# Kernel tuning notes

Measured on AMD Instinct MI355X. Metric: run time of the kernel, lower is better.

The kernel has to match this reference:

```python
import jax, jax.numpy as jnp
import numpy as np

H = 128  # hidden size
D = 257  # input size


def _lstm(x, h0, c0, Wih, Whh, bih, bhh):
    """Single-layer batch-first LSTM, PyTorch gate order (i, f, g, o).
    x: [N, T, D_in]; h0, c0: [N, H]. Returns (ys [N,T,H], hT, cT)."""
    # Precompute the input contribution for all timesteps at once.
    pre = jnp.einsum('ntd,gd->ntg', x, Wih) + bih + bhh  # [N, T, 4H]

    def step(carry, g_t):
        h, c = carry
        gates = g_t + h @ Whh.T  # [N, 4H]
        i, f, g, o = jnp.split(gates, 4, axis=-1)
        c = jax.nn.sigmoid(f) * c + jax.nn.sigmoid(i) * jnp.tanh(g)
        h = jax.nn.sigmoid(o) * jnp.tanh(c)
        return (h, c), h

    (hT, cT), ys = jax.lax.scan(step, (h0, c0), jnp.swapaxes(pre, 0, 1))
    return jnp.swapaxes(ys, 0, 1), hT, cT


def setup_inputs() -> dict:
    key = jax.random.key(0)
    ks = jax.random.split(key, 12)
    N, T = 64, 1000
    s1 = 1.0 / np.sqrt(H)
    inp = {
        'x': jax.random.normal(ks[0], (N, T, D), jnp.float32),
        'in_states': jax.random.normal(ks[1], (1, 4 * N, H), jnp.float32),
        'Wih1': jax.random.uniform(ks[2], (4 * H, D), jnp.float32, -s1, s1),
        'Whh1': jax.random.uniform(ks[3], (4 * H, H), jnp.float32, -s1, s1),
        'bih1': jax.random.uniform(ks[4], (4 * H,), jnp.float32, -s1, s1),
        'bhh1': jax.random.uniform(ks[5], (4 * H,), jnp.float32, -s1, s1),
        'Wih2': jax.random.uniform(ks[6], (4 * H, H), jnp.float32, -s1, s1),
        'Whh2': jax.random.uniform(ks[7], (4 * H, H), jnp.float32, -s1, s1),
        'bih2': jax.random.uniform(ks[8], (4 * H,), jnp.float32, -s1, s1),
        'bhh2': jax.random.uniform(ks[9], (4 * H,), jnp.float32, -s1, s1),
        'Wd': jax.random.uniform(ks[10], (D, H), jnp.float32, -s1, s1),
        'bd': jax.random.uniform(ks[11], (D,), jnp.float32, -s1, s1),
    }
    return inp


def reference(x, in_states, Wih1, Whh1, bih1, bhh1, Wih2, Whh2, bih2, bhh2, Wd, bd):
    # in_states: [1, 4N, H] -> four [1, N, H] chunks: h1, c1, h2, c2
    h1_in, c1_in, h2_in, c2_in = jnp.split(in_states, 4, axis=1)
    x1, h1, c1 = _lstm(x, h1_in[0], c1_in[0], Wih1, Whh1, bih1, bhh1)
    # dropout is identity in eval/streaming inference
    x2, h2, c2 = _lstm(x1, h2_in[0], c2_in[0], Wih2, Whh2, bih2, bhh2)
    mask = jax.nn.sigmoid(jnp.einsum('nth,dh->ntd', x2, Wd) + bd)
    out_states = jnp.concatenate([h1[None], c1[None], h2[None], c2[None]], axis=1)
    return mask, out_states
```

## Files before the change

### kernel.cpp

```cpp
#include <hip/hip_runtime.h>
#include <hip/hip_bf16.h>
#include <math.h>

#define NBATCH 64
#define TSEQ   1000
#define DIN    257
#define HID    128
#define GATES  512
#define CH     40
#define NCHUNK 25

typedef _Float16 h2    __attribute__((ext_vector_type(2)));
typedef _Float16 h4    __attribute__((ext_vector_type(4)));
typedef _Float16 half8 __attribute__((ext_vector_type(8)));
typedef float    f32x4 __attribute__((ext_vector_type(4)));

__device__ __forceinline__ float fast_sigmoid(float x) {
    return __builtin_amdgcn_rcpf(1.f + __expf(-x));
}
__device__ __forceinline__ float fast_tanh(float x) {
    const float e = __expf(2.f * x);
    return 1.f - 2.f * __builtin_amdgcn_rcpf(e + 1.f);
}
__device__ __forceinline__ void wait_flag(const int* f, int need) {
    while (__hip_atomic_load(f, __ATOMIC_ACQUIRE, __HIP_MEMORY_SCOPE_AGENT) < need)
        __builtin_amdgcn_s_sleep(2);
}
__device__ __forceinline__ half8 cvt8(const float* p) {
    const float4 a = *(const float4*)p;
    const float4 b = *(const float4*)(p + 4);
    half8 t;
    t[0] = (_Float16)a.x; t[1] = (_Float16)a.y;
    t[2] = (_Float16)a.z; t[3] = (_Float16)a.w;
    t[4] = (_Float16)b.x; t[5] = (_Float16)b.y;
    t[6] = (_Float16)b.z; t[7] = (_Float16)b.w;
    return t;
}

#define BM 128
#define BN 64
#define BK 64
#define LDK 88

template<int ACT>
__global__ __launch_bounds__(256) void gemm_mfma(
    const float* __restrict__ A, const float* __restrict__ W,
    const float* __restrict__ b1, const float* __restrict__ b2,
    float* __restrict__ C, int M, int K, int Ncols)
{
    __shared__ _Float16 As[BM][LDK];
    __shared__ _Float16 Ws[BN][LDK];

    const int tid  = threadIdx.x;
    const int wave = tid >> 6;
    const int lane = tid & 63;
    const int r    = lane & 15;
    const int q    = lane >> 4;
    const int m0   = blockIdx.y * BM;
    const int n0   = blockIdx.x * BN;
    const int wm   = (wave >> 1) * 64;
    const int wn   = (wave & 1) * 32;

    const int r16 = tid >> 4;
    const int c4  = (tid & 15) * 4;

    f32x4 acc[4][2];
#pragma unroll
    for (int i = 0; i < 4; ++i)
#pragma unroll
        for (int j = 0; j < 2; ++j) acc[i][j] = f32x4{0.f, 0.f, 0.f, 0.f};

    for (int kc = 0; kc < K; kc += BK) {
        const int kg = kc + c4;
        const bool vec_ok = (kg + 4 <= K);

#pragma unroll
        for (int it = 0; it < 8; ++it) {
            const int row = it * 16 + r16;
            const float* src = A + (size_t)(m0 + row) * K + kg;
            _Float16 tmp[4];
            if (vec_ok) {
                const float4 u = *(const float4*)src;
                tmp[0] = (_Float16)u.x; tmp[1] = (_Float16)u.y;
                tmp[2] = (_Float16)u.z; tmp[3] = (_Float16)u.w;
            } else {
#pragma unroll
                for (int j = 0; j < 4; ++j)
                    tmp[j] = (kg + j < K) ? (_Float16)src[j] : (_Float16)0.f;
            }
            *(h4*)&As[row][c4] = *(h4*)tmp;
        }
#pragma unroll
        for (int it = 0; it < 4; ++it) {
            const int row  = it * 16 + r16;
            const int wrow = n0 + row;
            _Float16 tmp[4] = {(_Float16)0.f, (_Float16)0.f, (_Float16)0.f, (_Float16)0.f};
            if (wrow < Ncols) {
                const float* src = W + (size_t)wrow * K + kg;
                if (vec_ok) {
                    const float4 u = *(const float4*)src;
                    tmp[0] = (_Float16)u.x; tmp[1] = (_Float16)u.y;
                    tmp[2] = (_Float16)u.z; tmp[3] = (_Float16)u.w;
                } else {
#pragma unroll
                    for (int j = 0; j < 4; ++j)
                        tmp[j] = (kg + j < K) ? (_Float16)src[j] : (_Float16)0.f;
                }
            }
            *(h4*)&Ws[row][c4] = *(h4*)tmp;
        }
        __syncthreads();

#pragma unroll
        for (int s = 0; s < 2; ++s) {
            const int kb = s * 32 + q * 8;
            half8 af[4], wfr[2];
#pragma unroll
            for (int i = 0; i < 4; ++i)
                af[i] = *(const half8*)&As[wm + i * 16 + r][kb];
#pragma unroll
            for (int j = 0; j < 2; ++j)
                wfr[j] = *(const half8*)&Ws[wn + j * 16 + r][kb];
#pragma unroll
            for (int i = 0; i < 4; ++i)
#pragma unroll
                for (int j = 0; j < 2; ++j)
                    acc[i][j] = __builtin_amdgcn_mfma_f32_16x16x32_f16(
                        af[i], wfr[j], acc[i][j], 0, 0, 0);
        }
        __syncthreads();
    }

#pragma unroll
    for (int i = 0; i < 4; ++i) {
#pragma unroll
        for (int j = 0; j < 2; ++j) {
            const int col = n0 + wn + j * 16 + r;
            if (col < Ncols) {
                const float bias = b1[col] + (b2 ? b2[col] : 0.f);
#pragma unroll
                for (int reg = 0; reg < 4; ++reg) {
                    const int row = m0 + wm + i * 16 + q * 4 + reg;
                    float v = acc[i][j][reg] + bias;
                    if (ACT == 1) v = fast_sigmoid(v);
                    C[(size_t)row * Ncols + col] = v;
                }
            }
        }
    }
}

__global__ __launch_bounds__(256, 1) void lstm_mega(
    const float* __restrict__ pre1, const float* __restrict__ states_in,
    const float* __restrict__ Whh1, const float* __restrict__ Whh2,
    const float* __restrict__ Wih2, const float* __restrict__ bih2,
    const float* __restrict__ bhh2,
    _Float16* __restrict__ h1g,
    float* __restrict__ h2seq,
    float* __restrict__ states_out, int* __restrict__ flags)
{
    const int layer = blockIdx.x >> 6;
    const int n     = blockIdx.x & 63;
    const int tid   = threadIdx.x;
    const int w     = tid >> 6;
    const int lane  = tid & 63;
    const int r     = lane & 15;
    const int q     = lane >> 4;
    const int b     = q & 1;
    const int j     = 32 * w + 16 * b + r;
    const int h_row0 = layer ? 128 : 0;

    __shared__ __align__(16) _Float16 hbuf[2][HID];
    __shared__ __align__(16) float pre2ck[CH][GATES + 4];

    const float* Whh = layer ? Whh2 : Whh1;
    half8 wf[4][2][4];
#pragma unroll
    for (int g = 0; g < 4; ++g)
#pragma unroll
        for (int b2 = 0; b2 < 2; ++b2) {
            const float* src = Whh + (size_t)(128 * g + 32 * w + 16 * b2 + r) * HID + q * 8;
#pragma unroll
            for (int s = 0; s < 4; ++s) wf[g][b2][s] = cvt8(src + s * 32);
        }

    half8 wih[8][4];
    float bias2v[8];
    if (layer == 1) {
#pragma unroll
        for (int fi = 0; fi < 8; ++fi) {
            const int row = 128 * w + 16 * fi + r;
            const float* src = Wih2 + (size_t)row * HID + q * 8;
#pragma unroll
            for (int s = 0; s < 4; ++s) wih[fi][s] = cvt8(src + s * 32);
            bias2v[fi] = bih2[row] + bhh2[row];
        }
    }

    float c_r = states_in[(size_t)(h_row0 + 64 + n) * HID + j];
    if (tid < HID)
        hbuf[0][tid] = (_Float16)states_in[(size_t)(h_row0 + n) * HID + tid];
    __syncthreads();

    const float* pre_n = pre1 + (size_t)n * TSEQ * GATES;
    float pc0 = 0.f, pc1 = 0.f, pc2 = 0.f, pc3 = 0.f;
    float pn0 = 0.f, pn1 = 0.f, pn2 = 0.f, pn3 = 0.f;
    if (layer == 0) {
        pc0 = pre_n[j];           pc1 = pre_n[j + 128];
        pc2 = pre_n[j + 256];     pc3 = pre_n[j + 384];
        pn0 = pre_n[GATES + j];       pn1 = pre_n[GATES + j + 128];
        pn2 = pre_n[GATES + j + 256]; pn3 = pre_n[GATES + j + 384];
    }

    const f32x4 Z = {0.f, 0.f, 0.f, 0.f};
    int cur = 0, ts = 0, ck = 0;

    for (int t = 0; t < TSEQ; ++t) {
        if (layer == 1 && ts == 0) {
            wait_flag(flags + n, ck + 1);
            const _Float16* hbase = h1g + ((size_t)n * TSEQ + (size_t)ck * CH) * HID;
#pragma unroll
            for (int mt = 0; mt < 3; ++mt) {
                const int mrow = (mt < 2) ? (mt * 16 + r) : (32 + (r & 7));
                const _Float16* src = hbase + (size_t)mrow * HID + q * 8;
                half8 ax[4];
#pragma unroll
                for (int s = 0; s < 4; ++s)
                    ax[s] = *(const half8*)(src + s * 32);
                f32x4 gacc[8];
#pragma unroll
                for (int fi = 0; fi < 8; ++fi)
                    gacc[fi] = __builtin_amdgcn_mfma_f32_16x16x32_f16(
                        ax[0], wih[fi][0], Z, 0, 0, 0);
#pragma unroll
                for (int s = 1; s < 4; ++s)
#pragma unroll
                    for (int fi = 0; fi < 8; ++fi)
                        gacc[fi] = __builtin_amdgcn_mfma_f32_16x16x32_f16(
                            ax[s], wih[fi][s], gacc[fi], 0, 0, 0);
                if (mt < 2 || q < 2) {
#pragma unroll
                    for (int fi = 0; fi < 8; ++fi)
#pragma unroll
                        for (int reg = 0; reg < 4; ++reg)
                            pre2ck[mt * 16 + 4 * q + reg][128 * w + 16 * fi + r] =
                                gacc[fi][reg] + bias2v[fi];
                }
            }
            __syncthreads();
        }

        float p0, p1, p2, p3;
        if (layer == 0) {
            p0 = pc0; p1 = pc1; p2 = pc2; p3 = pc3;
            pc0 = pn0; pc1 = pn1; pc2 = pn2; pc3 = pn3;
            if (t + 2 < TSEQ) {
                const float* pp = pre_n + (size_t)(t + 2) * GATES + j;
                pn0 = pp[0]; pn1 = pp[128]; pn2 = pp[256]; pn3 = pp[384];
            }
        } else {
            p0 = pre2ck[ts][j];
            p1 = pre2ck[ts][j + 128];
            p2 = pre2ck[ts][j + 256];
            p3 = pre2ck[ts][j + 384];
        }

        half8 hx[4];
#pragma unroll
        for (int s = 0; s < 4; ++s)
            hx[s] = *(const half8*)&hbuf[cur][s * 32 + q * 8];

        f32x4 acc[4][2];
#pragma unroll
        for (int g = 0; g < 4; ++g)
#pragma unroll
            for (int b2 = 0; b2 < 2; ++b2)
                acc[g][b2] = __builtin_amdgcn_mfma_f32_16x16x32_f16(
                    hx[0], wf[g][b2][0], Z, 0, 0, 0);
#pragma unroll
        for (int s = 1; s < 4; ++s)
#pragma unroll
            for (int g = 0; g < 4; ++g)
#pragma unroll
                for (int b2 = 0; b2 < 2; ++b2)
                    acc[g][b2] = __builtin_amdgcn_mfma_f32_16x16x32_f16(
                        hx[s], wf[g][b2][s], acc[g][b2], 0, 0, 0);

        const float A0 = (b ? acc[0][1][0] : acc[0][0][0]) + p0;
        const float A1 = (b ? acc[1][1][0] : acc[1][0][0]) + p1;
        const float A2 = (b ? acc[2][1][0] : acc[2][0][0]) + p2;
        const float A3 = (b ? acc[3][1][0] : acc[3][0][0]) + p3;

        const float gi = fast_sigmoid(A0);
        const float gf = fast_sigmoid(A1);
        const float gg = fast_tanh(A2);
        const float go = fast_sigmoid(A3);

        const float cn = gf * c_r + gi * gg;
        const float hh = go * fast_tanh(cn);
        c_r = cn;

        if (q < 2) {
            hbuf[cur ^ 1][j] = (_Float16)hh;
            if (t == TSEQ - 1)
                states_out[(size_t)(h_row0 + 64 + n) * HID + j] = cn;
        } else {
            if (layer == 0)
                h1g[((size_t)n * TSEQ + t) * HID + j] = (_Float16)hh;
            else
                h2seq[((size_t)n * TSEQ + t) * HID + j] = hh;
            if (t == TSEQ - 1)
                states_out[(size_t)(h_row0 + n) * HID + j] = hh;
        }
        __syncthreads();

        if (layer == 0 && ts == CH - 1 && tid == 0) {
            __threadfence();
            __hip_atomic_store(flags + n, ck + 1,
                               __ATOMIC_RELAXED, __HIP_MEMORY_SCOPE_AGENT);
        }

        if (++ts == CH) { ts = 0; ++ck; }
        cur ^= 1;
    }
}

extern "C" void kernel_launch(void* const* d_in, const int* in_sizes, int n_in,
                              void* d_out, int out_size, void* d_ws, size_t ws_size,
                              hipStream_t stream)
{
    const float* x     = (const float*)d_in[0];
    const float* st_in = (const float*)d_in[1];
    const float* Wih1  = (const float*)d_in[2];
    const float* Whh1  = (const float*)d_in[3];
    const float* bih1  = (const float*)d_in[4];
    const float* bhh1  = (const float*)d_in[5];
    const float* Wih2  = (const float*)d_in[6];
    const float* Whh2  = (const float*)d_in[7];
    const float* bih2  = (const float*)d_in[8];
    const float* bhh2  = (const float*)d_in[9];
    const float* Wd    = (const float*)d_in[10];
    const float* bd    = (const float*)d_in[11];

    float* out_mask   = (float*)d_out;
    float* out_states = (float*)d_out + (size_t)NBATCH * TSEQ * DIN;

    const int M = NBATCH * TSEQ;
    float* bufA = (float*)d_ws;
    float* bufB = bufA + (size_t)M * GATES;

    _Float16* h1g = (_Float16*)out_mask;
    int* flags = (int*)(out_mask + (size_t)NBATCH * TSEQ * DIN) - 64;
    hipMemsetAsync(flags, 0, 64 * sizeof(int), stream);

    gemm_mfma<0><<<dim3(GATES / BN, M / BM), 256, 0, stream>>>(
        x, Wih1, bih1, bhh1, bufA, M, DIN, GATES);

    lstm_mega<<<128, 256, 0, stream>>>(
        bufA, st_in, Whh1, Whh2, Wih2, bih2, bhh2, h1g, bufB, out_states, flags);

    gemm_mfma<1><<<dim3((DIN + BN - 1) / BN, M / BM), 256, 0, stream>>>(
        bufB, Wd, bd, nullptr, out_mask, M, HID, DIN);
}
```

Measured before the change: 1.097 ms.

## Fuse mask projection GEMM into layer-2 LSTM blocks per chunk

Removes the final mask GEMM launch and the fp32 h2 sequence round-trip through global memory. Layer-2 blocks now keep each 40-step chunk of h2 in LDS as fp16, hold an fp16 swizzled copy of Wd in LDS, and compute and store sigmoid masks with MFMA at the start of the next chunk. The h1 staging buffer moves from the output region to workspace, and its stores become nontemporal. The cost is more LDS use and extra work on the layer-2 path. All four waves appear to redo the same mask computation and write identical outputs.

```diff
diff --git a/kernel.cpp b/kernel.cpp
--- a/kernel.cpp
+++ b/kernel.cpp
@@ -155,8 +155,9 @@
     const float* __restrict__ Whh1, const float* __restrict__ Whh2,
     const float* __restrict__ Wih2, const float* __restrict__ bih2,
     const float* __restrict__ bhh2,
+    const float* __restrict__ Wd, const float* __restrict__ bd,
     _Float16* __restrict__ h1g,
-    float* __restrict__ h2seq,
+    float* __restrict__ mask_out,
     float* __restrict__ states_out, int* __restrict__ flags)
 {
     const int layer = blockIdx.x >> 6;
@@ -171,7 +172,9 @@
     const int h_row0 = layer ? 128 : 0;
 
     __shared__ __align__(16) _Float16 hbuf[2][HID];
-    __shared__ __align__(16) float pre2ck[CH][GATES + 4];
+    __shared__ __align__(16) float    pre2ck[CH][GATES + 4];
+    __shared__ __align__(16) _Float16 wd_lds[272][HID];
+    __shared__ __align__(16) _Float16 h2ck[CH][136];
 
     const float* Whh = layer ? Whh2 : Whh1;
     half8 wf[4][2][4];
@@ -194,6 +197,16 @@
 #pragma unroll
             for (int s = 0; s < 4; ++s) wih[fi][s] = cvt8(src + s * 32);
             bias2v[fi] = bih2[row] + bhh2[row];
+        }
+        for (int i = tid; i < 15 * HID; i += 256)
+            wd_lds[257 + (i >> 7)][i & 127] = (_Float16)0.f;
+        for (int i = tid; i < 257 * 32; i += 256) {
+            const int row = i >> 5, c4 = (i & 31) * 4;
+            const float4 u = *(const float4*)(Wd + (size_t)row * HID + c4);
+            _Float16 t4[4] = {(_Float16)u.x, (_Float16)u.y,
+                              (_Float16)u.z, (_Float16)u.w};
+            const int byte = row * 256 + ((c4 * 2) ^ ((row & 7) << 4));
+            *(h4*)((char*)&wd_lds[0][0] + byte) = *(h4*)t4;
         }
     }
 
@@ -213,10 +226,50 @@
     }
 
     const f32x4 Z = {0.f, 0.f, 0.f, 0.f};
+
+    auto mask_fold = [&](int c) {
+#pragma unroll
+        for (int mt = 0; mt < 3; ++mt) {
+            const int mrow = (mt < 2) ? (mt * 16 + r) : (32 + (r & 7));
+            half8 ax[4];
+#pragma unroll
+            for (int s = 0; s < 4; ++s)
+                ax[s] = *(const half8*)&h2ck[mrow][s * 32 + q * 8];
+#pragma unroll
+            for (int fi = 0; fi < 17; ++fi) {
+                const int wrow = 16 * fi + r;
+                half8 wb[4];
+#pragma unroll
+                for (int s = 0; s < 4; ++s) {
+                    const int byte = wrow * 256 +
+                        ((s * 64 + q * 16) ^ ((wrow & 7) << 4));
+                    wb[s] = *(const half8*)((const char*)&wd_lds[0][0] + byte);
+                }
+                f32x4 g = __builtin_amdgcn_mfma_f32_16x16x32_f16(
+                    ax[0], wb[0], Z, 0, 0, 0);
+#pragma unroll
+                for (int s = 1; s < 4; ++s)
+                    g = __builtin_amdgcn_mfma_f32_16x16x32_f16(
+                        ax[s], wb[s], g, 0, 0, 0);
+                if (wrow < DIN && (mt < 2 || q < 2)) {
+                    const float bias = bd[wrow];
+#pragma unroll
+                    for (int reg = 0; reg < 4; ++reg) {
+                        const int tt = c * CH + mt * 16 + 4 * q + reg;
+                        __builtin_nontemporal_store(
+                            fast_sigmoid(g[reg] + bias),
+                            mask_out + ((size_t)n * TSEQ + tt) * DIN + wrow);
+                    }
+                }
+            }
+        }
+    };
+
     int cur = 0, ts = 0, ck = 0;
 
     for (int t = 0; t < TSEQ; ++t) {
         if (layer == 1 && ts == 0) {
+            if (ck > 0) mask_fold(ck - 1);
             wait_flag(flags + n, ck + 1);
             const _Float16* hbase = h1g + ((size_t)n * TSEQ + (size_t)ck * CH) * HID;
 #pragma unroll
@@ -306,9 +359,10 @@
                 states_out[(size_t)(h_row0 + 64 + n) * HID + j] = cn;
         } else {
             if (layer == 0)
-                h1g[((size_t)n * TSEQ + t) * HID + j] = (_Float16)hh;
+                __builtin_nontemporal_store((_Float16)hh,
+                    &h1g[((size_t)n * TSEQ + t) * HID + j]);
             else
-                h2seq[((size_t)n * TSEQ + t) * HID + j] = hh;
+                h2ck[ts][j] = (_Float16)hh;
             if (t == TSEQ - 1)
                 states_out[(size_t)(h_row0 + n) * HID + j] = hh;
         }
@@ -323,6 +377,8 @@
         if (++ts == CH) { ts = 0; ++ck; }
         cur ^= 1;
     }
+
+    if (layer == 1) mask_fold(NCHUNK - 1);
 }
 
 extern "C" void kernel_launch(void* const* d_in, const int* in_sizes, int n_in,
@@ -349,16 +405,14 @@
     float* bufA = (float*)d_ws;
     float* bufB = bufA + (size_t)M * GATES;
 
-    _Float16* h1g = (_Float16*)out_mask;
-    int* flags = (int*)(out_mask + (size_t)NBATCH * TSEQ * DIN) - 64;
+    _Float16* h1g = (_Float16*)bufB;
+    int* flags = (int*)(bufB + (size_t)M * (HID / 2));
     hipMemsetAsync(flags, 0, 64 * sizeof(int), stream);
 
     gemm_mfma<0><<<dim3(GATES / BN, M / BM), 256, 0, stream>>>(
         x, Wih1, bih1, bhh1, bufA, M, DIN, GATES);
 
     lstm_mega<<<128, 256, 0, stream>>>(
-        bufA, st_in, Whh1, Whh2, Wih2, bih2, bhh2, h1g, bufB, out_states, flags);
-
-    gemm_mfma<1><<<dim3((DIN + BN - 1) / BN, M / BM), 256, 0, stream>>>(
-        bufB, Wd, bd, nullptr, out_mask, M, HID, DIN);
-}
+        bufA, st_in, Whh1, Whh2, Wih2, bih2, bhh2, Wd, bd,
+        h1g, out_mask, out_states, flags);
+}
```

After: 2.050 ms. +86.8%, slower.

## Batch 16 sequences per block and pipeline layer-2 input projection in separate blocks

Applied to the files above, without the earlier changes.

Restructures the recurrent LSTM kernel so each 512-thread block advances 16 batch chains together, using the full 16 rows of each MFMA instead of one sequence per block. A swizzled LDS h buffer avoids bank conflicts. The layer-2 input projection moves into 64 dedicated producer blocks that write pre-activations back into the layer-1 buffer, synchronised through two flag arrays, so the layer-2 recurrence only consumes precomputed values. This cuts per-step work and barrier count per sequence, but adds inter-block flag waits and more global-memory traffic for the layer-2 pre-activations.

```diff
diff --git a/kernel.cpp b/kernel.cpp
--- a/kernel.cpp
+++ b/kernel.cpp
@@ -7,8 +7,9 @@
 #define DIN    257
 #define HID    128
 #define GATES  512
-#define CH     40
+#define CHK    40
 #define NCHUNK 25
+#define GPC    16
 
 typedef _Float16 h2    __attribute__((ext_vector_type(2)));
 typedef _Float16 h4    __attribute__((ext_vector_type(4)));
@@ -150,178 +151,187 @@
     }
 }
 
-__global__ __launch_bounds__(256, 1) void lstm_mega(
-    const float* __restrict__ pre1, const float* __restrict__ states_in,
+__global__ __launch_bounds__(512, 1) void lstm_pipe(
+    float* preA,
+    const float* __restrict__ states_in,
     const float* __restrict__ Whh1, const float* __restrict__ Whh2,
     const float* __restrict__ Wih2, const float* __restrict__ bih2,
     const float* __restrict__ bhh2,
-    _Float16* __restrict__ h1g,
+    _Float16* h1g,
     float* __restrict__ h2seq,
-    float* __restrict__ states_out, int* __restrict__ flags)
+    float* __restrict__ states_out,
+    int* flag1, int* flag2)
 {
-    const int layer = blockIdx.x >> 6;
-    const int n     = blockIdx.x & 63;
-    const int tid   = threadIdx.x;
-    const int w     = tid >> 6;
-    const int lane  = tid & 63;
-    const int r     = lane & 15;
-    const int q     = lane >> 4;
-    const int b     = q & 1;
-    const int j     = 32 * w + 16 * b + r;
-    const int h_row0 = layer ? 128 : 0;
-
-    __shared__ __align__(16) _Float16 hbuf[2][HID];
-    __shared__ __align__(16) float pre2ck[CH][GATES + 4];
-
-    const float* Whh = layer ? Whh2 : Whh1;
-    half8 wf[4][2][4];
-#pragma unroll
-    for (int g = 0; g < 4; ++g)
-#pragma unroll
-        for (int b2 = 0; b2 < 2; ++b2) {
-            const float* src = Whh + (size_t)(128 * g + 32 * w + 16 * b2 + r) * HID + q * 8;
-#pragma unroll
-            for (int s = 0; s < 4; ++s) wf[g][b2][s] = cvt8(src + s * 32);
-        }
-
-    half8 wih[8][4];
-    float bias2v[8];
-    if (layer == 1) {
-#pragma unroll
-        for (int fi = 0; fi < 8; ++fi) {
-            const int row = 128 * w + 16 * fi + r;
+    const int bid  = blockIdx.x;
+    const int tid  = threadIdx.x;
+    const int u    = tid >> 6;
+    const int lane = tid & 63;
+    const int r    = lane & 15;
+    const int q    = lane >> 4;
+    const f32x4 Z  = {0.f, 0.f, 0.f, 0.f};
+
+    __shared__ _Float16 hbuf[2][GPC * HID];
+
+    if (bid >= 4 && bid < 68) {
+        const int n = bid - 4, grp = n >> 4;
+        half8 wih[4][4];
+        float bias2v[4];
+#pragma unroll
+        for (int fi = 0; fi < 4; ++fi) {
+            const int row = 16 * (4 * u + fi) + r;
             const float* src = Wih2 + (size_t)row * HID + q * 8;
 #pragma unroll
             for (int s = 0; s < 4; ++s) wih[fi][s] = cvt8(src + s * 32);
             bias2v[fi] = bih2[row] + bhh2[row];
         }
-    }
-
-    float c_r = states_in[(size_t)(h_row0 + 64 + n) * HID + j];
-    if (tid < HID)
-        hbuf[0][tid] = (_Float16)states_in[(size_t)(h_row0 + n) * HID + tid];
-    __syncthreads();
-
-    const float* pre_n = pre1 + (size_t)n * TSEQ * GATES;
-    float pc0 = 0.f, pc1 = 0.f, pc2 = 0.f, pc3 = 0.f;
-    float pn0 = 0.f, pn1 = 0.f, pn2 = 0.f, pn3 = 0.f;
-    if (layer == 0) {
-        pc0 = pre_n[j];           pc1 = pre_n[j + 128];
-        pc2 = pre_n[j + 256];     pc3 = pre_n[j + 384];
-        pn0 = pre_n[GATES + j];       pn1 = pre_n[GATES + j + 128];
-        pn2 = pre_n[GATES + j + 256]; pn3 = pre_n[GATES + j + 384];
-    }
-
-    const f32x4 Z = {0.f, 0.f, 0.f, 0.f};
-    int cur = 0, ts = 0, ck = 0;
-
-    for (int t = 0; t < TSEQ; ++t) {
-        if (layer == 1 && ts == 0) {
-            wait_flag(flags + n, ck + 1);
-            const _Float16* hbase = h1g + ((size_t)n * TSEQ + (size_t)ck * CH) * HID;
+        for (int ck = 0; ck < NCHUNK; ++ck) {
+            wait_flag(flag1 + grp, ck + 1);
+            const _Float16* hbase = h1g + ((size_t)n * TSEQ + ck * CHK) * HID;
+            float* pbase = preA + ((size_t)n * TSEQ + ck * CHK) * GATES;
 #pragma unroll
             for (int mt = 0; mt < 3; ++mt) {
-                const int mrow = (mt < 2) ? (mt * 16 + r) : (32 + (r & 7));
+                const int mrow = (mt < 2) ? mt * 16 + r : 32 + (r & 7);
                 const _Float16* src = hbase + (size_t)mrow * HID + q * 8;
                 half8 ax[4];
 #pragma unroll
-                for (int s = 0; s < 4; ++s)
-                    ax[s] = *(const half8*)(src + s * 32);
-                f32x4 gacc[8];
-#pragma unroll
-                for (int fi = 0; fi < 8; ++fi)
+                for (int s = 0; s < 4; ++s) ax[s] = *(const half8*)(src + s * 32);
+                f32x4 gacc[4];
+#pragma unroll
+                for (int fi = 0; fi < 4; ++fi)
                     gacc[fi] = __builtin_amdgcn_mfma_f32_16x16x32_f16(
                         ax[0], wih[fi][0], Z, 0, 0, 0);
 #pragma unroll
                 for (int s = 1; s < 4; ++s)
 #pragma unroll
-                    for (int fi = 0; fi < 8; ++fi)
+                    for (int fi = 0; fi < 4; ++fi)
                         gacc[fi] = __builtin_amdgcn_mfma_f32_16x16x32_f16(
                             ax[s], wih[fi][s], gacc[fi], 0, 0, 0);
                 if (mt < 2 || q < 2) {
 #pragma unroll
-                    for (int fi = 0; fi < 8; ++fi)
+                    for (int fi = 0; fi < 4; ++fi)
 #pragma unroll
                         for (int reg = 0; reg < 4; ++reg)
-                            pre2ck[mt * 16 + 4 * q + reg][128 * w + 16 * fi + r] =
-                                gacc[fi][reg] + bias2v[fi];
+                            pbase[(size_t)(mt * 16 + 4 * q + reg) * GATES +
+                                  16 * (4 * u + fi) + r] = gacc[fi][reg] + bias2v[fi];
                 }
             }
             __syncthreads();
-        }
-
-        float p0, p1, p2, p3;
-        if (layer == 0) {
-            p0 = pc0; p1 = pc1; p2 = pc2; p3 = pc3;
-            pc0 = pn0; pc1 = pn1; pc2 = pn2; pc3 = pn3;
-            if (t + 2 < TSEQ) {
-                const float* pp = pre_n + (size_t)(t + 2) * GATES + j;
-                pn0 = pp[0]; pn1 = pp[128]; pn2 = pp[256]; pn3 = pp[384];
-            }
-        } else {
-            p0 = pre2ck[ts][j];
-            p1 = pre2ck[ts][j + 128];
-            p2 = pre2ck[ts][j + 256];
-            p3 = pre2ck[ts][j + 384];
-        }
+            if (tid == 0) {
+                __threadfence();
+                __hip_atomic_store(flag2 + n, ck + 1,
+                                   __ATOMIC_RELAXED, __HIP_MEMORY_SCOPE_AGENT);
+            }
+        }
+        return;
+    }
+
+    const int layer  = (bid >= 68) ? 1 : 0;
+    const int grp    = layer ? bid - 68 : bid;
+    const int h_row0 = layer ? 128 : 0;
+    const int j      = 16 * u + r;
+    const int n0     = 16 * grp + 4 * q;
+    const float* Whh = layer ? Whh2 : Whh1;
+
+    half8 wf[4][4];
+#pragma unroll
+    for (int g = 0; g < 4; ++g) {
+        const float* src = Whh + (size_t)(128 * g + j) * HID + q * 8;
+#pragma unroll
+        for (int s = 0; s < 4; ++s) wf[g][s] = cvt8(src + s * 32);
+    }
+
+    float c_r[4];
+#pragma unroll
+    for (int reg = 0; reg < 4; ++reg)
+        c_r[reg] = states_in[(size_t)(h_row0 + 64 + n0 + reg) * HID + j];
+    for (int i = tid; i < GPC * HID; i += 512) {
+        const int chain = i >> 7, jj = i & 127;
+        const float v = states_in[(size_t)(h_row0 + 16 * grp + chain) * HID + jj];
+        const int byte = chain * 256 + ((2 * jj) ^ ((chain & 7) << 4));
+        *(_Float16*)((char*)&hbuf[0][0] + byte) = (_Float16)v;
+    }
+    __syncthreads();
+
+    auto ldp = [&](int tt, float (&P)[4][4]) {
+#pragma unroll
+        for (int reg = 0; reg < 4; ++reg) {
+            const float* pp = preA + ((size_t)(n0 + reg) * TSEQ + tt) * GATES + j;
+#pragma unroll
+            for (int g = 0; g < 4; ++g) P[g][reg] = pp[128 * g];
+        }
+    };
+
+    if (layer) {
+        wait_flag(flag2 + 16 * grp + (tid & 15), NCHUNK < 2 ? NCHUNK : 2);
+        __syncthreads();
+    }
+
+    float pA_[4][4], pB_[4][4];
+    ldp(0, pA_);
+    ldp(1, pB_);
+
+    int cur = 0;
+
+    auto step = [&](int t, float (&P)[4][4]) {
+        f32x4 acc[4];
+#pragma unroll
+        for (int g = 0; g < 4; ++g)
+            acc[g] = f32x4{P[g][0], P[g][1], P[g][2], P[g][3]};
+        if (t + 2 < TSEQ) ldp(t + 2, P);
 
         half8 hx[4];
 #pragma unroll
+        for (int s = 0; s < 4; ++s) {
+            const int byte = r * 256 + ((s * 64 + q * 16) ^ ((r & 7) << 4));
+            hx[s] = *(const half8*)((const char*)&hbuf[cur][0] + byte);
+        }
+#pragma unroll
         for (int s = 0; s < 4; ++s)
-            hx[s] = *(const half8*)&hbuf[cur][s * 32 + q * 8];
-
-        f32x4 acc[4][2];
-#pragma unroll
-        for (int g = 0; g < 4; ++g)
-#pragma unroll
-            for (int b2 = 0; b2 < 2; ++b2)
-                acc[g][b2] = __builtin_amdgcn_mfma_f32_16x16x32_f16(
-                    hx[0], wf[g][b2][0], Z, 0, 0, 0);
-#pragma unroll
-        for (int s = 1; s < 4; ++s)
 #pragma unroll
             for (int g = 0; g < 4; ++g)
-#pragma unroll
-                for (int b2 = 0; b2 < 2; ++b2)
-                    acc[g][b2] = __builtin_amdgcn_mfma_f32_16x16x32_f16(
-                        hx[s], wf[g][b2][s], acc[g][b2], 0, 0, 0);
-
-        const float A0 = (b ? acc[0][1][0] : acc[0][0][0]) + p0;
-        const float A1 = (b ? acc[1][1][0] : acc[1][0][0]) + p1;
-        const float A2 = (b ? acc[2][1][0] : acc[2][0][0]) + p2;
-        const float A3 = (b ? acc[3][1][0] : acc[3][0][0]) + p3;
-
-        const float gi = fast_sigmoid(A0);
-        const float gf = fast_sigmoid(A1);
-        const float gg = fast_tanh(A2);
-        const float go = fast_sigmoid(A3);
-
-        const float cn = gf * c_r + gi * gg;
-        const float hh = go * fast_tanh(cn);
-        c_r = cn;
-
-        if (q < 2) {
-            hbuf[cur ^ 1][j] = (_Float16)hh;
-            if (t == TSEQ - 1)
-                states_out[(size_t)(h_row0 + 64 + n) * HID + j] = cn;
-        } else {
+                acc[g] = __builtin_amdgcn_mfma_f32_16x16x32_f16(
+                    hx[s], wf[g][s], acc[g], 0, 0, 0);
+
+#pragma unroll
+        for (int reg = 0; reg < 4; ++reg) {
+            const float gi = fast_sigmoid(acc[0][reg]);
+            const float gf = fast_sigmoid(acc[1][reg]);
+            const float gg = fast_tanh(acc[2][reg]);
+            const float go = fast_sigmoid(acc[3][reg]);
+            const float cn = gf * c_r[reg] + gi * gg;
+            const float hh = go * fast_tanh(cn);
+            c_r[reg] = cn;
+            const int row  = 4 * q + reg;
+            const int byte = row * 256 + ((2 * j) ^ ((row & 7) << 4));
+            *(_Float16*)((char*)&hbuf[cur ^ 1][0] + byte) = (_Float16)hh;
             if (layer == 0)
-                h1g[((size_t)n * TSEQ + t) * HID + j] = (_Float16)hh;
+                h1g[((size_t)(n0 + reg) * TSEQ + t) * HID + j] = (_Float16)hh;
             else
-                h2seq[((size_t)n * TSEQ + t) * HID + j] = hh;
-            if (t == TSEQ - 1)
-                states_out[(size_t)(h_row0 + n) * HID + j] = hh;
+                h2seq[((size_t)(n0 + reg) * TSEQ + t) * HID + j] = hh;
+            if (t == TSEQ - 1) {
+                states_out[(size_t)(h_row0 + n0 + reg) * HID + j]      = hh;
+                states_out[(size_t)(h_row0 + 64 + n0 + reg) * HID + j] = cn;
+            }
         }
         __syncthreads();
 
-        if (layer == 0 && ts == CH - 1 && tid == 0) {
+        if (layer == 0 && (t % CHK) == CHK - 1 && tid == 0) {
             __threadfence();
-            __hip_atomic_store(flags + n, ck + 1,
+            __hip_atomic_store(flag1 + grp, t / CHK + 1,
                                __ATOMIC_RELAXED, __HIP_MEMORY_SCOPE_AGENT);
         }
-
-        if (++ts == CH) { ts = 0; ++ck; }
         cur ^= 1;
+    };
+
+    for (int t = 0; t < TSEQ; t += 2) {
+        if (layer && t > 0 && (t % CHK) == 0) {
+            const int ck = t / CHK;
+            const int need = (ck + 2 < NCHUNK) ? ck + 2 : NCHUNK;
+            wait_flag(flag2 + 16 * grp + (tid & 15), need);
+            __syncthreads();
+        }
+        step(t, pA_);
+        step(t + 1, pB_);
     }
 }
 
@@ -350,14 +360,17 @@
     float* bufB = bufA + (size_t)M * GATES;
 
     _Float16* h1g = (_Float16*)out_mask;
-    int* flags = (int*)(out_mask + (size_t)NBATCH * TSEQ * DIN) - 64;
-    hipMemsetAsync(flags, 0, 64 * sizeof(int), stream);
+    int* fbase = (int*)(out_mask + (size_t)NBATCH * TSEQ * DIN) - 128;
+    int* flag1 = fbase;
+    int* flag2 = fbase + 4;
+    hipMemsetAsync(fbase, 0, 128 * sizeof(int), stream);
 
     gemm_mfma<0><<<dim3(GATES / BN, M / BM), 256, 0, stream>>>(
         x, Wih1, bih1, bhh1, bufA, M, DIN, GATES);
 
-    lstm_mega<<<128, 256, 0, stream>>>(
-        bufA, st_in, Whh1, Whh2, Wih2, bih2, bhh2, h1g, bufB, out_states, flags);
+    lstm_pipe<<<72, 512, 0, stream>>>(
+        bufA, st_in, Whh1, Whh2, Wih2, bih2, bhh2,
+        h1g, bufB, out_states, flag1, flag2);
 
     gemm_mfma<1><<<dim3((DIN + BN - 1) / BN, M / BM), 256, 0, stream>>>(
         bufB, Wd, bd, nullptr, out_mask, M, HID, DIN);
```

Result: slower. 2.021 ms (+84.2%).

## Pre-convert GEMM operands to padded fp16 and store layer-2 hidden sequence as fp16

Applied to the files above, without the earlier changes.

Adds a conversion kernel that turns x, Wih1 and Wd into fp16 copies, with x and Wih1 zero-padded to K=320, so the GEMM loads half8 vectors with no bounds checks or per-tile conversion. The LSTM now writes the layer-2 hidden sequence in fp16, which halves that write and the read in the output GEMM. In exchange there are extra conversion passes over x (a full read plus a write of the padded fp16 copy), and more padded K work in the first GEMM. Scratch buffers are placed in the output and workspace regions, with xh and h1g packed into the mask buffer before the final GEMM overwrites it.

```diff
diff --git a/kernel.cpp b/kernel.cpp
--- a/kernel.cpp
+++ b/kernel.cpp
@@ -9,6 +9,7 @@
 #define GATES  512
 #define CH     40
 #define NCHUNK 25
+#define KP1    320
 
 typedef _Float16 h2    __attribute__((ext_vector_type(2)));
 typedef _Float16 h4    __attribute__((ext_vector_type(4)));
@@ -37,16 +38,46 @@
     return t;
 }
 
+__global__ __launch_bounds__(256) void cvt_rows(
+    const float* __restrict__ src, _Float16* __restrict__ dst,
+    int nrows, int sk, int dk)
+{
+    const int lane   = threadIdx.x & 63;
+    const int wid    = (blockIdx.x * 256 + threadIdx.x) >> 6;
+    const int nw     = (gridDim.x * 256) >> 6;
+    for (int row = wid; row < nrows; row += nw) {
+        for (int c0 = 0; c0 < dk; c0 += 256) {
+            const int c = c0 + lane * 4;
+            if (c >= dk) continue;
+            if (c + 4 <= sk) {
+                const float4 u = *(const float4*)(src + (size_t)row * sk + c);
+                h4 t; t[0] = (_Float16)u.x; t[1] = (_Float16)u.y;
+                      t[2] = (_Float16)u.z; t[3] = (_Float16)u.w;
+                *(h4*)(dst + (size_t)row * dk + c) = t;
+            } else {
+#pragma unroll
+                for (int jj = 0; jj < 4; ++jj) {
+                    const int cc = c + jj;
+                    if (cc < dk)
+                        dst[(size_t)row * dk + cc] =
+                            (cc < sk) ? (_Float16)src[(size_t)row * sk + cc]
+                                      : (_Float16)0.f;
+                }
+            }
+        }
+    }
+}
+
 #define BM 128
 #define BN 64
 #define BK 64
 #define LDK 88
 
 template<int ACT>
-__global__ __launch_bounds__(256) void gemm_mfma(
-    const float* __restrict__ A, const float* __restrict__ W,
+__global__ __launch_bounds__(256) void gemm_f16(
+    const _Float16* __restrict__ A, const _Float16* __restrict__ W,
     const float* __restrict__ b1, const float* __restrict__ b2,
-    float* __restrict__ C, int M, int K, int Ncols)
+    float* __restrict__ C, int M, int Ka, int Ncols)
 {
     __shared__ _Float16 As[BM][LDK];
     __shared__ _Float16 Ws[BN][LDK];
@@ -61,8 +92,8 @@
     const int wm   = (wave >> 1) * 64;
     const int wn   = (wave & 1) * 32;
 
-    const int r16 = tid >> 4;
-    const int c4  = (tid & 15) * 4;
+    const int r32 = tid >> 3;
+    const int c8  = (tid & 7) * 8;
 
     f32x4 acc[4][2];
 #pragma unroll
@@ -70,44 +101,21 @@
 #pragma unroll
         for (int j = 0; j < 2; ++j) acc[i][j] = f32x4{0.f, 0.f, 0.f, 0.f};
 
-    for (int kc = 0; kc < K; kc += BK) {
-        const int kg = kc + c4;
-        const bool vec_ok = (kg + 4 <= K);
-
-#pragma unroll
-        for (int it = 0; it < 8; ++it) {
-            const int row = it * 16 + r16;
-            const float* src = A + (size_t)(m0 + row) * K + kg;
-            _Float16 tmp[4];
-            if (vec_ok) {
-                const float4 u = *(const float4*)src;
-                tmp[0] = (_Float16)u.x; tmp[1] = (_Float16)u.y;
-                tmp[2] = (_Float16)u.z; tmp[3] = (_Float16)u.w;
-            } else {
-#pragma unroll
-                for (int j = 0; j < 4; ++j)
-                    tmp[j] = (kg + j < K) ? (_Float16)src[j] : (_Float16)0.f;
-            }
-            *(h4*)&As[row][c4] = *(h4*)tmp;
-        }
+    for (int kc = 0; kc < Ka; kc += BK) {
 #pragma unroll
         for (int it = 0; it < 4; ++it) {
-            const int row  = it * 16 + r16;
+            const int row = it * 32 + r32;
+            *(half8*)&As[row][c8] =
+                *(const half8*)(A + (size_t)(m0 + row) * Ka + kc + c8);
+        }
+#pragma unroll
+        for (int it = 0; it < 2; ++it) {
+            const int row  = it * 32 + r32;
             const int wrow = n0 + row;
-            _Float16 tmp[4] = {(_Float16)0.f, (_Float16)0.f, (_Float16)0.f, (_Float16)0.f};
-            if (wrow < Ncols) {
-                const float* src = W + (size_t)wrow * K + kg;
-                if (vec_ok) {
-                    const float4 u = *(const float4*)src;
-                    tmp[0] = (_Float16)u.x; tmp[1] = (_Float16)u.y;
-                    tmp[2] = (_Float16)u.z; tmp[3] = (_Float16)u.w;
-                } else {
-#pragma unroll
-                    for (int j = 0; j < 4; ++j)
-                        tmp[j] = (kg + j < K) ? (_Float16)src[j] : (_Float16)0.f;
-                }
-            }
-            *(h4*)&Ws[row][c4] = *(h4*)tmp;
+            half8 t = {};
+            if (wrow < Ncols)
+                t = *(const half8*)(W + (size_t)wrow * Ka + kc + c8);
+            *(half8*)&Ws[row][c8] = t;
         }
         __syncthreads();
 
@@ -156,7 +164,7 @@
     const float* __restrict__ Wih2, const float* __restrict__ bih2,
     const float* __restrict__ bhh2,
     _Float16* __restrict__ h1g,
-    float* __restrict__ h2seq,
+    _Float16* __restrict__ h2seq,
     float* __restrict__ states_out, int* __restrict__ flags)
 {
     const int layer = blockIdx.x >> 6;
@@ -308,7 +316,7 @@
             if (layer == 0)
                 h1g[((size_t)n * TSEQ + t) * HID + j] = (_Float16)hh;
             else
-                h2seq[((size_t)n * TSEQ + t) * HID + j] = hh;
+                h2seq[((size_t)n * TSEQ + t) * HID + j] = (_Float16)hh;
             if (t == TSEQ - 1)
                 states_out[(size_t)(h_row0 + n) * HID + j] = hh;
         }
@@ -349,16 +357,25 @@
     float* bufA = (float*)d_ws;
     float* bufB = bufA + (size_t)M * GATES;
 
-    _Float16* h1g = (_Float16*)out_mask;
+    _Float16* h2seq = (_Float16*)bufB;
+    _Float16* wih1h = h2seq + (size_t)M * HID;
+    _Float16* wdh   = wih1h + (size_t)GATES * KP1;
+
+    _Float16* xh  = (_Float16*)out_mask;
+    _Float16* h1g = xh + (size_t)M * KP1;
     int* flags = (int*)(out_mask + (size_t)NBATCH * TSEQ * DIN) - 64;
     hipMemsetAsync(flags, 0, 64 * sizeof(int), stream);
 
-    gemm_mfma<0><<<dim3(GATES / BN, M / BM), 256, 0, stream>>>(
-        x, Wih1, bih1, bhh1, bufA, M, DIN, GATES);
+    cvt_rows<<<256, 256, 0, stream>>>(x,    xh,    M,     DIN, KP1);
+    cvt_rows<<<8,   256, 0, stream>>>(Wih1, wih1h, GATES, DIN, KP1);
+    cvt_rows<<<8,   256, 0, stream>>>(Wd,   wdh,   DIN,   HID, HID);
+
+    gemm_f16<0><<<dim3(GATES / BN, M / BM), 256, 0, stream>>>(
+        xh, wih1h, bih1, bhh1, bufA, M, KP1, GATES);
 
     lstm_mega<<<128, 256, 0, stream>>>(
-        bufA, st_in, Whh1, Whh2, Wih2, bih2, bhh2, h1g, bufB, out_states, flags);
-
-    gemm_mfma<1><<<dim3((DIN + BN - 1) / BN, M / BM), 256, 0, stream>>>(
-        bufB, Wd, bd, nullptr, out_mask, M, HID, DIN);
-}
+        bufA, st_in, Whh1, Whh2, Wih2, bih2, bhh2, h1g, h2seq, out_states, flags);
+
+    gemm_f16<1><<<dim3((DIN + BN - 1) / BN, M / BM), 256, 0, stream>>>(
+        h2seq, wdh, bd, nullptr, out_mask, M, HID, DIN);
+}
```

New measurement: 1.071 ms. 2.4% less time.
